# Performance work log

Measured on AMD Instinct MI355X. Metric: run time of the kernel, lower is better.

Reference implementation:

```python
import jax, jax.numpy as jnp
import numpy as np
from jax import lax

V, E, H, K = 50257, 256, 256, 3
T, B, S = 1024, 32, 1024


def setup_inputs() -> dict:
    key = jax.random.key(0)
    ks = jax.random.split(key, 10)
    inp = {
        "source": jax.random.randint(ks[0], (T, B), 0, V),
        "target": jax.random.randint(ks[1], (T, B), 0, V),
        "enc_attn": jax.random.normal(ks[2], (B, S, H), jnp.float32),
        "source_seq_out": jax.random.normal(ks[3], (B, S, 2 * H), jnp.float32),
        "emb": jax.random.normal(ks[4], (V, E), jnp.float32) * 0.02,
        "affine_w": jax.random.normal(ks[5], (2 * H, E), jnp.float32) * 0.02,
        "affine_b": jnp.zeros((2 * H,), jnp.float32),
        "conv_w": jax.random.normal(ks[6], (2 * H, 1, K, 2 * H), jnp.float32) * 0.02,
        "conv_b": jnp.zeros((2 * H,), jnp.float32),
        "map_w": jax.random.normal(ks[7], (2 * H, H), jnp.float32) * 0.02,
        "map_b": jnp.zeros((2 * H,), jnp.float32),
    }
    return inp


def reference(source, target, enc_attn, source_seq_out, emb, affine_w, affine_b,
              conv_w, conv_b, map_w, map_b):
    # source is unused by the original forward (kept for signature fidelity)
    x = emb[target]                                   # [T, B, E]
    x = x @ affine_w.T + affine_b                     # [T, B, 2H]
    x = jnp.transpose(x, (1, 0, 2))                   # [B, T, 2H]  (.t() swaps dims 0,1)
    x = x[:, None, :, :]                              # [B, 1, T, 2H]
    # conv2d: out_ch=2H, kernel=(K, 2H), padding=(K-1, 0) -> [B, 2H, T+K-1, 1]
    y = lax.conv_general_dilated(
        x, conv_w, window_strides=(1, 1),
        padding=((K - 1, K - 1), (0, 0)),
        dimension_numbers=("NCHW", "OIHW", "NCHW"))
    y = y + conv_b[None, :, None, None]
    y = y[:, :, : y.shape[2] - K, :]                  # narrow -> length L = T - 1 (faithful)
    y = jax.nn.relu(y)
    y = jnp.transpose(y[..., 0], (0, 2, 1))           # [B, L, 2H]
    A, Bg = y[..., :H], y[..., H:]                    # GLU split
    dec_attn = A * jax.nn.softmax(Bg, axis=-1)        # [B, L, H]
    dec_attn2 = dec_attn @ map_w.T + map_b            # [B, L, 2H]
    scores = jnp.einsum("blh,bsh->bls", dec_attn, enc_attn)   # [B, L, S]
    attn = jax.nn.softmax(scores, axis=-1)
    attns = jnp.einsum("bls,bsd->bld", attn, source_seq_out)  # [B, L, 2H]
    return dec_attn2 + attns
```

## Files before the change

kernel.cpp:

```cpp
#include <hip/hip_runtime.h>
#include <stdint.h>


typedef __bf16 bf16x8_t __attribute__((ext_vector_type(8)));
typedef float  f32x4_t  __attribute__((ext_vector_type(4)));

#define DEV __device__ __forceinline__

DEV unsigned short f2bf(float f) {
  union { float f; unsigned u; } v; v.f = f;
  unsigned r = v.u + 0x7fffu + ((v.u >> 16) & 1u);
  return (unsigned short)(r >> 16);
}
DEV float bf2f(unsigned short u) {
  union { unsigned u; float f; } v; v.u = ((unsigned)u) << 16;
  return v.f;
}

DEV void gload_lds16(const void* g, void* l) {
  __builtin_amdgcn_global_load_lds((const __attribute__((address_space(1))) void*)g,
                                   (__attribute__((address_space(3))) void*)l, 16, 0, 0);
}

__global__ void zero_k(unsigned short* p) { p[threadIdx.x] = 0; }

__global__ __launch_bounds__(256) void zero_rows_k(float* p) {
  int i = (blockIdx.x * 256 + threadIdx.x) * 4;
  *(float4*)(p + i) = make_float4(0.f, 0.f, 0.f, 0.f);
}

__global__ __launch_bounds__(256) void cvt_bf16_k(const float* __restrict__ src,
                                                  unsigned short* __restrict__ dst,
                                                  int n) {
  int i = (blockIdx.x * 256 + threadIdx.x) * 4;
  if (i >= n) return;
  float4 v = *(const float4*)(src + i);
  ushort4 o;
  o.x = f2bf(v.x); o.y = f2bf(v.y); o.z = f2bf(v.z); o.w = f2bf(v.w);
  *(ushort4*)(dst + i) = o;
}

__global__ __launch_bounds__(256) void cvt_transpose_v_k(const float* __restrict__ src,
                                                         unsigned short* __restrict__ dst) {
  __shared__ float tile[32][33];
  int b = blockIdx.z, s0 = blockIdx.x * 32, d0 = blockIdx.y * 32;
  int tx = threadIdx.x & 31, ty = threadIdx.x >> 5;
  const float* p = src + ((size_t)b * 1024 + s0) * 512 + d0;
  for (int r = ty; r < 32; r += 8) tile[r][tx] = p[(size_t)r * 512 + tx];
  __syncthreads();
  unsigned short* q = dst + ((size_t)b * 512 + d0) * 1024 + s0;
  for (int r = ty; r < 32; r += 8) q[(size_t)r * 1024 + tx] = f2bf(tile[tx][r]);
}

__global__ __launch_bounds__(256) void embed_affine_k(const int* __restrict__ tgt,
                                                      const float* __restrict__ emb,
                                                      const unsigned short* __restrict__ awb,
                                                      const float* __restrict__ ab,
                                                      unsigned short* __restrict__ X) {
  constexpr int AP = 264;
  __shared__ unsigned short xs[32 * AP];
  const int r0 = blockIdx.x * 32;
  const int tid = threadIdx.x;
  for (int idx = tid; idx < 32 * 64; idx += 256) {
    int r = idx >> 6, c4 = (idx & 63) * 4;
    int row = tgt[r0 + r];
    float4 v = *(const float4*)&emb[(size_t)row * 256 + c4];
    ushort4 o;
    o.x = f2bf(v.x); o.y = f2bf(v.y); o.z = f2bf(v.z); o.w = f2bf(v.w);
    *(ushort4*)&xs[r * AP + c4] = o;
  }
  __syncthreads();
  const int lane = tid & 63, w = tid >> 6, q = lane >> 4, ln = lane & 15;
  f32x4_t acc[2][8];
#pragma unroll
  for (int mt = 0; mt < 2; ++mt)
#pragma unroll
    for (int nt = 0; nt < 8; ++nt) acc[mt][nt] = (f32x4_t){0.f, 0.f, 0.f, 0.f};
  for (int kk = 0; kk < 256; kk += 32) {
    bf16x8_t a[2], bb[8];
#pragma unroll
    for (int mt = 0; mt < 2; ++mt)
      a[mt] = *(const bf16x8_t*)(xs + (mt * 16 + ln) * AP + kk + q * 8);
#pragma unroll
    for (int nt = 0; nt < 8; ++nt) {
      int n = ((w * 8 + nt) << 4) + ln;
      bb[nt] = *(const bf16x8_t*)(awb + ((size_t)n << 8) + kk + q * 8);
    }
#pragma unroll
    for (int mt = 0; mt < 2; ++mt)
#pragma unroll
      for (int nt = 0; nt < 8; ++nt)
        acc[mt][nt] = __builtin_amdgcn_mfma_f32_16x16x32_bf16(a[mt], bb[nt], acc[mt][nt], 0, 0, 0);
  }
#pragma unroll
  for (int nt = 0; nt < 8; ++nt) {
    const int o = ((w * 8 + nt) << 4) + ln;
    const float bias = ab[o];
#pragma unroll
    for (int mt = 0; mt < 2; ++mt)
#pragma unroll
      for (int r = 0; r < 4; ++r) {
        int rid = r0 + mt * 16 + q * 4 + r;
        int t = rid >> 5, b = rid & 31;
        X[(((size_t)(b * 1024 + t)) << 9) + o] = f2bf(acc[mt][nt][r] + bias);
      }
  }
}

DEV void cstage(unsigned short* AsB, unsigned short* BsB,
                const unsigned short* __restrict__ X,
                const unsigned short* __restrict__ Wc,
                const unsigned short* __restrict__ zbuf,
                int b, int l0, int n0, int t, int w, int srow, int scolg) {
  const int kk = t << 5;
  const int i  = kk >> 9;
  const int c0 = kk & 511;
  {
    const int lr = l0 + srow + i - 2;
    const unsigned short* sp = (lr < 0)
        ? (zbuf + scolg * 8)
        : (X + (((size_t)(b * 1024 + lr)) << 9) + c0 + scolg * 8);
    gload_lds16(sp, AsB + w * 512);
  }
  {
    const int lr = l0 + 64 + srow + i - 2;
    gload_lds16(X + (((size_t)(b * 1024 + lr)) << 9) + c0 + scolg * 8,
                AsB + 2048 + w * 512);
  }
  gload_lds16(Wc + (size_t)(n0 + srow) * 1536 + kk + scolg * 8, BsB + w * 512);
  gload_lds16(Wc + (size_t)(n0 + 64 + srow) * 1536 + kk + scolg * 8,
              BsB + 2048 + w * 512);
}

__global__ __launch_bounds__(256) void conv_gemm_k(const unsigned short* __restrict__ X,
                                                   const unsigned short* __restrict__ Wc,
                                                   const float* __restrict__ cb,
                                                   const unsigned short* __restrict__ zbuf,
                                                   unsigned short* __restrict__ Y) {
  __shared__ unsigned short As[2][4096];
  __shared__ unsigned short Bs[2][4096];
  const int bid = blockIdx.x;
  const int mtile = bid >> 2;
  const int b  = mtile >> 3;
  const int l0 = (mtile & 7) << 7;
  const int n0 = (bid & 3) << 7;
  const int tid = threadIdx.x;
  const int w = tid >> 6, lane = tid & 63, q = lane >> 4, ln = lane & 15;
  const int wr = w >> 1, wc = w & 1;
  const int srow = tid >> 2, scolg = tid & 3;

  f32x4_t acc[4][4];
#pragma unroll
  for (int mt = 0; mt < 4; ++mt)
#pragma unroll
    for (int nt = 0; nt < 4; ++nt) acc[mt][nt] = (f32x4_t){0.f, 0.f, 0.f, 0.f};

  cstage(As[0], Bs[0], X, Wc, zbuf, b, l0, n0, 0, w, srow, scolg);
  __syncthreads();

  for (int t = 0; t < 48; ++t) {
    const int cur = t & 1;
    if (t < 47)
      cstage(As[cur ^ 1], Bs[cur ^ 1], X, Wc, zbuf, b, l0, n0, t + 1, w, srow, scolg);
    const unsigned short* Ab = As[cur];
    const unsigned short* Bb = Bs[cur];
    bf16x8_t af[4], bf[4];
#pragma unroll
    for (int x = 0; x < 4; ++x) {
      af[x] = *(const bf16x8_t*)(Ab + (wr * 64 + x * 16 + ln) * 32 + q * 8);
      bf[x] = *(const bf16x8_t*)(Bb + (wc * 64 + x * 16 + ln) * 32 + q * 8);
    }
#pragma unroll
    for (int mt = 0; mt < 4; ++mt)
#pragma unroll
      for (int nt = 0; nt < 4; ++nt)
        acc[mt][nt] = __builtin_amdgcn_mfma_f32_16x16x32_bf16(af[mt], bf[nt], acc[mt][nt], 0, 0, 0);
    __syncthreads();
  }

#pragma unroll
  for (int nt = 0; nt < 4; ++nt) {
    const int o = n0 + wc * 64 + nt * 16 + ln;
    const float bias = cb[o];
#pragma unroll
    for (int mt = 0; mt < 4; ++mt)
#pragma unroll
      for (int r = 0; r < 4; ++r) {
        const int l = l0 + wr * 64 + mt * 16 + q * 4 + r;
        float v = acc[mt][nt][r] + bias;
        Y[(((size_t)b * 1024 + l) << 9) + o] = f2bf(v > 0.f ? v : 0.f);
      }
  }
}

__global__ __launch_bounds__(256) void glu_k(const unsigned short* __restrict__ Y,
                                             unsigned short* __restrict__ dec) {
  const int row = blockIdx.x * 4 + (threadIdx.x >> 6);
  const int lane = threadIdx.x & 63;
  const unsigned short* p = Y + ((size_t)row << 9);
  ushort4 av = *(const ushort4*)(p + lane * 4);
  ushort4 gv = *(const ushort4*)(p + 256 + lane * 4);
  float e0 = __expf(bf2f(gv.x)), e1 = __expf(bf2f(gv.y));
  float e2 = __expf(bf2f(gv.z)), e3 = __expf(bf2f(gv.w));
  float s = e0 + e1 + e2 + e3;
#pragma unroll
  for (int off = 32; off > 0; off >>= 1) s += __shfl_xor(s, off);
  float inv = 1.f / s;
  ushort4 o;
  o.x = f2bf(bf2f(av.x) * e0 * inv);
  o.y = f2bf(bf2f(av.y) * e1 * inv);
  o.z = f2bf(bf2f(av.z) * e2 * inv);
  o.w = f2bf(bf2f(av.w) * e3 * inv);
  *(ushort4*)(dec + ((size_t)row << 8) + lane * 4) = o;
}

DEV void gstage(unsigned short* AsB, unsigned short* BsB,
                const unsigned short* __restrict__ Arow,
                const unsigned short* __restrict__ Brow,
                int strideA, int strideB, int kk, int w, int srow, int scolg) {
  gload_lds16(Arow + (size_t)srow * strideA + kk + scolg * 8, AsB + w * 512);
  gload_lds16(Arow + (size_t)(64 + srow) * strideA + kk + scolg * 8,
              AsB + 2048 + w * 512);
  gload_lds16(Brow + (size_t)srow * strideB + kk + scolg * 8, BsB + w * 512);
  gload_lds16(Brow + (size_t)(64 + srow) * strideB + kk + scolg * 8,
              BsB + 2048 + w * 512);
}

__global__ __launch_bounds__(256) void attn_s_k(const unsigned short* __restrict__ dec,
                                                const unsigned short* __restrict__ enc,
                                                unsigned short* __restrict__ P,
                                                float* __restrict__ rows) {
  __shared__ unsigned short As[2][4096];
  __shared__ unsigned short Bs[2][4096];
  const int bid = blockIdx.x;
  const int wg = ((bid & 7) << 8) + (bid >> 3);
  const int ntile = wg & 7, mtile = wg >> 3;
  const int b = mtile >> 3;
  const int row0 = mtile << 7;
  const int s0 = ntile << 7;
  const int tid = threadIdx.x;
  const int w = tid >> 6, lane = tid & 63, q = lane >> 4, ln = lane & 15;
  const int wr = w >> 1, wc = w & 1;
  const int srow = tid >> 2, scolg = tid & 3;

  const unsigned short* Ab = dec + ((size_t)row0 << 8);
  const unsigned short* Bb = enc + ((size_t)b << 18) + ((size_t)s0 << 8);

  f32x4_t acc[4][4];
#pragma unroll
  for (int mt = 0; mt < 4; ++mt)
#pragma unroll
    for (int nt = 0; nt < 4; ++nt) acc[mt][nt] = (f32x4_t){0.f, 0.f, 0.f, 0.f};

  gstage(As[0], Bs[0], Ab, Bb, 256, 256, 0, w, srow, scolg);
  __syncthreads();

  for (int t = 0; t < 8; ++t) {
    const int cur = t & 1;
    if (t < 7)
      gstage(As[cur ^ 1], Bs[cur ^ 1], Ab, Bb, 256, 256, (t + 1) << 5, w, srow, scolg);
    const unsigned short* Ap = As[cur];
    const unsigned short* Bp = Bs[cur];
    bf16x8_t af[4], bf[4];
#pragma unroll
    for (int x = 0; x < 4; ++x) {
      af[x] = *(const bf16x8_t*)(Ap + (wr * 64 + x * 16 + ln) * 32 + q * 8);
      bf[x] = *(const bf16x8_t*)(Bp + (wc * 64 + x * 16 + ln) * 32 + q * 8);
    }
#pragma unroll
    for (int mt = 0; mt < 4; ++mt)
#pragma unroll
      for (int nt = 0; nt < 4; ++nt)
        acc[mt][nt] = __builtin_amdgcn_mfma_f32_16x16x32_bf16(af[mt], bf[nt], acc[mt][nt], 0, 0, 0);
    __syncthreads();
  }

  float rs[4][4];
#pragma unroll
  for (int mt = 0; mt < 4; ++mt)
#pragma unroll
    for (int r = 0; r < 4; ++r) rs[mt][r] = 0.f;
#pragma unroll
  for (int nt = 0; nt < 4; ++nt) {
    const int col = s0 + wc * 64 + nt * 16 + ln;
#pragma unroll
    for (int mt = 0; mt < 4; ++mt)
#pragma unroll
      for (int r = 0; r < 4; ++r) {
        const int row = row0 + wr * 64 + mt * 16 + q * 4 + r;
        float e = __expf(acc[mt][nt][r]);
        rs[mt][r] += e;
        P[((size_t)row << 10) + col] = f2bf(e);
      }
  }
#pragma unroll
  for (int mt = 0; mt < 4; ++mt)
#pragma unroll
    for (int r = 0; r < 4; ++r) {
      float v = rs[mt][r];
      v += __shfl_xor(v, 1); v += __shfl_xor(v, 2);
      v += __shfl_xor(v, 4); v += __shfl_xor(v, 8);
      if (ln == 0)
        atomicAdd(&rows[row0 + wr * 64 + mt * 16 + q * 4 + r], v);
    }
}

__global__ __launch_bounds__(256) void attn_pv_k(const unsigned short* __restrict__ P,
                                                 const unsigned short* __restrict__ vt,
                                                 const unsigned short* __restrict__ dec,
                                                 const unsigned short* __restrict__ mw,
                                                 const float* __restrict__ rows,
                                                 const float* __restrict__ mb,
                                                 float* __restrict__ out) {
  __shared__ unsigned short As[2][4096];
  __shared__ unsigned short Bs[2][4096];
  const int bid = blockIdx.x;
  const int wg = ((bid & 7) << 7) + (bid >> 3);
  const int ntile = wg & 3, mtile = wg >> 2;
  const int b = mtile >> 3;
  const int row0 = mtile << 7;
  const int d0 = ntile << 7;
  const int tid = threadIdx.x;
  const int w = tid >> 6, lane = tid & 63, q = lane >> 4, ln = lane & 15;
  const int wr = w >> 1, wc = w & 1;
  const int srow = tid >> 2, scolg = tid & 3;

  const unsigned short* A1 = P + ((size_t)row0 << 10);
  const unsigned short* B1 = vt + ((size_t)b << 19) + ((size_t)d0 << 10);
  const unsigned short* A2 = dec + ((size_t)row0 << 8);
  const unsigned short* B2 = mw + ((size_t)d0 << 8);

  float rinv[4][4];
#pragma unroll
  for (int mt = 0; mt < 4; ++mt)
#pragma unroll
    for (int r = 0; r < 4; ++r)
      rinv[mt][r] = 1.f / rows[row0 + wr * 64 + mt * 16 + q * 4 + r];

  f32x4_t acc[4][4];
#pragma unroll
  for (int mt = 0; mt < 4; ++mt)
#pragma unroll
    for (int nt = 0; nt < 4; ++nt) acc[mt][nt] = (f32x4_t){0.f, 0.f, 0.f, 0.f};

  gstage(As[0], Bs[0], A1, B1, 1024, 1024, 0, w, srow, scolg);
  __syncthreads();

  for (int t = 0; t < 40; ++t) {
    const int cur = t & 1;
    if (t < 39) {
      const int tn = t + 1;
      if (tn < 32)
        gstage(As[cur ^ 1], Bs[cur ^ 1], A1, B1, 1024, 1024, tn << 5, w, srow, scolg);
      else
        gstage(As[cur ^ 1], Bs[cur ^ 1], A2, B2, 256, 256, (tn - 32) << 5, w, srow, scolg);
    }
    const unsigned short* Ap = As[cur];
    const unsigned short* Bp = Bs[cur];
    bf16x8_t af[4], bf[4];
#pragma unroll
    for (int x = 0; x < 4; ++x) {
      af[x] = *(const bf16x8_t*)(Ap + (wr * 64 + x * 16 + ln) * 32 + q * 8);
      bf[x] = *(const bf16x8_t*)(Bp + (wc * 64 + x * 16 + ln) * 32 + q * 8);
    }
#pragma unroll
    for (int mt = 0; mt < 4; ++mt)
#pragma unroll
      for (int nt = 0; nt < 4; ++nt)
        acc[mt][nt] = __builtin_amdgcn_mfma_f32_16x16x32_bf16(af[mt], bf[nt], acc[mt][nt], 0, 0, 0);
    if (t == 31) {
#pragma unroll
      for (int mt = 0; mt < 4; ++mt)
#pragma unroll
        for (int nt = 0; nt < 4; ++nt)
#pragma unroll
          for (int r = 0; r < 4; ++r) acc[mt][nt][r] *= rinv[mt][r];
    }
    __syncthreads();
  }

#pragma unroll
  for (int nt = 0; nt < 4; ++nt) {
    const int d = d0 + wc * 64 + nt * 16 + ln;
    const float bias = mb[d];
#pragma unroll
    for (int mt = 0; mt < 4; ++mt)
#pragma unroll
      for (int r = 0; r < 4; ++r) {
        const int row = row0 + wr * 64 + mt * 16 + q * 4 + r;
        const int l = row & 1023;
        if (l < 1023)
          out[((size_t)b * 1023 + l) * 512 + d] = acc[mt][nt][r] + bias;
      }
  }
}

extern "C" void kernel_launch(void* const* d_in, const int* in_sizes, int n_in,
                              void* d_out, int out_size, void* d_ws, size_t ws_size,
                              hipStream_t stream) {
  const int*   target = (const int*)d_in[1];
  const float* enc    = (const float*)d_in[2];
  const float* src    = (const float*)d_in[3];
  const float* emb    = (const float*)d_in[4];
  const float* aw     = (const float*)d_in[5];
  const float* ab     = (const float*)d_in[6];
  const float* cw     = (const float*)d_in[7];
  const float* cb     = (const float*)d_in[8];
  const float* mw     = (const float*)d_in[9];
  const float* mb     = (const float*)d_in[10];
  float* out = (float*)d_out;
  char* ws = (char*)d_ws;

  unsigned short* Xbf  = (unsigned short*)(ws);
  unsigned short* Ybf  = (unsigned short*)(ws + 33554432);
  unsigned short* Pb   = (unsigned short*)(ws);
  unsigned short* dec  = (unsigned short*)(ws + 67108864);
  unsigned short* encb = (unsigned short*)(ws + 83886080);
  unsigned short* vtb  = (unsigned short*)(ws + 100663296);
  unsigned short* wcb  = (unsigned short*)(ws + 134217728);
  float*          rows = (float*)(ws + 134217728);
  unsigned short* mwb  = (unsigned short*)(ws + 135790592);
  unsigned short* awb  = (unsigned short*)(ws + 136052736);

  zero_k<<<1, 512, 0, stream>>>(dec);
  cvt_bf16_k<<<8192, 256, 0, stream>>>(enc, encb, 32 * 1024 * 256);
  cvt_bf16_k<<<768, 256, 0, stream>>>(cw, wcb, 512 * 1536);
  cvt_bf16_k<<<128, 256, 0, stream>>>(mw, mwb, 512 * 256);
  cvt_bf16_k<<<128, 256, 0, stream>>>(aw, awb, 512 * 256);
  cvt_transpose_v_k<<<dim3(32, 16, 32), 256, 0, stream>>>(src, vtb);
  embed_affine_k<<<1024, 256, 0, stream>>>(target, emb, awb, ab, Xbf);
  conv_gemm_k<<<1024, 256, 0, stream>>>(Xbf, wcb, cb, dec, Ybf);
  zero_rows_k<<<32, 256, 0, stream>>>(rows);
  glu_k<<<8192, 256, 0, stream>>>(Ybf, dec);
  attn_s_k<<<2048, 256, 0, stream>>>(dec, encb, Pb, rows);
  attn_pv_k<<<1024, 256, 0, stream>>>(Pb, vtb, dec, mwb, rows, mb, out);
}
```

Before: 452.5 us.

## Triple-buffer GEMM kernels with vmcnt barriers, LDS swizzle, and wider transpose

Replaces the double-buffered LDS staging in the conv, attention-score and PV GEMM kernels with a three-stage ring buffer. Each step waits with partial vmcnt counts instead of a full __syncthreads, so two global-to-LDS loads stay in flight. Adds an XOR swizzle on LDS columns to cut bank conflicts, raises MFMA priority with s_setprio, and remaps conv block indices for L2 locality. The V transpose kernel now uses 64x64 tiles with float4 loads and 16-byte bf16 stores. The extra LDS per block (48KB) may limit occupancy, and the hand-written waitcnt counts must match the number of loads issued per stage exactly.

```diff
diff --git a/kernel.cpp b/kernel.cpp
--- a/kernel.cpp
+++ b/kernel.cpp
@@ -4,6 +4,7 @@
 
 typedef __bf16 bf16x8_t __attribute__((ext_vector_type(8)));
 typedef float  f32x4_t  __attribute__((ext_vector_type(4)));
+typedef unsigned short u16x8 __attribute__((ext_vector_type(8)));
 
 #define DEV __device__ __forceinline__
 
@@ -20,6 +21,38 @@
 DEV void gload_lds16(const void* g, void* l) {
   __builtin_amdgcn_global_load_lds((const __attribute__((address_space(1))) void*)g,
                                    (__attribute__((address_space(3))) void*)l, 16, 0, 0);
+}
+
+DEV void vm_bar8() { asm volatile("s_waitcnt vmcnt(8)" ::: "memory"); __builtin_amdgcn_s_barrier(); }
+DEV void vm_bar4() { asm volatile("s_waitcnt vmcnt(4)" ::: "memory"); __builtin_amdgcn_s_barrier(); }
+DEV void vm_bar0() { asm volatile("s_waitcnt vmcnt(0)" ::: "memory"); __builtin_amdgcn_s_barrier(); }
+DEV void lgkm_bar() { asm volatile("s_waitcnt lgkmcnt(0)" ::: "memory"); __builtin_amdgcn_s_barrier(); }
+
+DEV void stage32(unsigned short* Ld, int tid,
+                 const unsigned short* a0, const unsigned short* a1,
+                 const unsigned short* b0, const unsigned short* b1, int tt) {
+  const int o = tt * 32;
+  gload_lds16(a0 + o, Ld + tid * 8);
+  gload_lds16(a1 + o, Ld + (tid + 256) * 8);
+  gload_lds16(b0 + o, Ld + 4096 + tid * 8);
+  gload_lds16(b1 + o, Ld + 4096 + (tid + 256) * 8);
+}
+
+DEV void gemm_step32(const unsigned short* Ld, int wr, int wc, int ln, int qsw,
+                     f32x4_t (&acc)[4][4]) {
+  bf16x8_t af[4], bff[4];
+#pragma unroll
+  for (int x = 0; x < 4; ++x) {
+    af[x]  = *(const bf16x8_t*)(Ld + (wr * 64 + x * 16 + ln) * 32 + qsw);
+    bff[x] = *(const bf16x8_t*)(Ld + 4096 + (wc * 64 + x * 16 + ln) * 32 + qsw);
+  }
+  __builtin_amdgcn_s_setprio(1);
+#pragma unroll
+  for (int mt = 0; mt < 4; ++mt)
+#pragma unroll
+    for (int nt = 0; nt < 4; ++nt)
+      acc[mt][nt] = __builtin_amdgcn_mfma_f32_16x16x32_bf16(af[mt], bff[nt], acc[mt][nt], 0, 0, 0);
+  __builtin_amdgcn_s_setprio(0);
 }
 
 __global__ void zero_k(unsigned short* p) { p[threadIdx.x] = 0; }
@@ -42,14 +75,30 @@
 
 __global__ __launch_bounds__(256) void cvt_transpose_v_k(const float* __restrict__ src,
                                                          unsigned short* __restrict__ dst) {
-  __shared__ float tile[32][33];
-  int b = blockIdx.z, s0 = blockIdx.x * 32, d0 = blockIdx.y * 32;
-  int tx = threadIdx.x & 31, ty = threadIdx.x >> 5;
+  __shared__ float tile[64][65];
+  const int b = blockIdx.z, s0 = blockIdx.x * 64, d0 = blockIdx.y * 64;
+  const int tid = threadIdx.x;
+  const int cs = (tid & 15) * 4;
+  const int rs = tid >> 4;
   const float* p = src + ((size_t)b * 1024 + s0) * 512 + d0;
-  for (int r = ty; r < 32; r += 8) tile[r][tx] = p[(size_t)r * 512 + tx];
+#pragma unroll
+  for (int rr = 0; rr < 4; ++rr) {
+    const int s = rs + rr * 16;
+    float4 v = *(const float4*)(p + (size_t)s * 512 + cs);
+    tile[s][cs] = v.x; tile[s][cs + 1] = v.y;
+    tile[s][cs + 2] = v.z; tile[s][cs + 3] = v.w;
+  }
   __syncthreads();
-  unsigned short* q = dst + ((size_t)b * 512 + d0) * 1024 + s0;
-  for (int r = ty; r < 32; r += 8) q[(size_t)r * 1024 + tx] = f2bf(tile[tx][r]);
+  const int ch = tid & 7;
+  const int dd0 = tid >> 3;
+#pragma unroll
+  for (int it = 0; it < 2; ++it) {
+    const int dd = dd0 + it * 32;
+    u16x8 o;
+#pragma unroll
+    for (int j = 0; j < 8; ++j) o[j] = f2bf(tile[ch * 8 + j][dd]);
+    *(u16x8*)(dst + ((size_t)b * 512 + d0 + dd) * 1024 + s0 + ch * 8) = o;
+  }
 }
 
 __global__ __launch_bounds__(256) void embed_affine_k(const int* __restrict__ tgt,
@@ -107,47 +156,45 @@
   }
 }
 
-DEV void cstage(unsigned short* AsB, unsigned short* BsB,
-                const unsigned short* __restrict__ X,
-                const unsigned short* __restrict__ Wc,
-                const unsigned short* __restrict__ zbuf,
-                int b, int l0, int n0, int t, int w, int srow, int scolg) {
-  const int kk = t << 5;
-  const int i  = kk >> 9;
-  const int c0 = kk & 511;
-  {
-    const int lr = l0 + srow + i - 2;
-    const unsigned short* sp = (lr < 0)
-        ? (zbuf + scolg * 8)
-        : (X + (((size_t)(b * 1024 + lr)) << 9) + c0 + scolg * 8);
-    gload_lds16(sp, AsB + w * 512);
-  }
-  {
-    const int lr = l0 + 64 + srow + i - 2;
-    gload_lds16(X + (((size_t)(b * 1024 + lr)) << 9) + c0 + scolg * 8,
-                AsB + 2048 + w * 512);
-  }
-  gload_lds16(Wc + (size_t)(n0 + srow) * 1536 + kk + scolg * 8, BsB + w * 512);
-  gload_lds16(Wc + (size_t)(n0 + 64 + srow) * 1536 + kk + scolg * 8,
-              BsB + 2048 + w * 512);
-}
-
-__global__ __launch_bounds__(256) void conv_gemm_k(const unsigned short* __restrict__ X,
-                                                   const unsigned short* __restrict__ Wc,
-                                                   const float* __restrict__ cb,
-                                                   const unsigned short* __restrict__ zbuf,
-                                                   unsigned short* __restrict__ Y) {
-  __shared__ unsigned short As[2][4096];
-  __shared__ unsigned short Bs[2][4096];
+__global__ __launch_bounds__(256, 3) void conv_gemm_k(const unsigned short* __restrict__ X,
+                                                      const unsigned short* __restrict__ Wc,
+                                                      const float* __restrict__ cb,
+                                                      const unsigned short* __restrict__ zbuf,
+                                                      unsigned short* __restrict__ Y) {
+  __shared__ unsigned short tb[3][8192];
   const int bid = blockIdx.x;
-  const int mtile = bid >> 2;
+  const int mtile = ((bid >> 5) << 3) | (bid & 7);
+  const int ntile = (bid >> 3) & 3;
   const int b  = mtile >> 3;
   const int l0 = (mtile & 7) << 7;
-  const int n0 = (bid & 3) << 7;
+  const int n0 = ntile << 7;
   const int tid = threadIdx.x;
   const int w = tid >> 6, lane = tid & 63, q = lane >> 4, ln = lane & 15;
   const int wr = w >> 1, wc = w & 1;
-  const int srow = tid >> 2, scolg = tid & 3;
+  const int qsw = (q ^ (ln & 3)) << 3;
+
+  const int r0g = tid >> 2, r1g = (tid + 256) >> 2;
+  const int cg = tid & 3;
+  const int c0g = ((cg ^ (r0g & 3)) << 3);
+  const int c1g = ((cg ^ (r1g & 3)) << 3);
+
+  const unsigned short* Xb = X + ((size_t)b << 19);
+  const int lr0 = l0 + r0g - 2;
+  const int lr1 = l0 + r1g - 2;
+  const int tmin0 = (lr0 >= 0) ? 0 : (lr0 == -1 ? 16 : 32);
+  const unsigned short* a0 = Xb + ((long)lr0 * 512 + c0g);
+  const unsigned short* a1 = Xb + ((long)lr1 * 512 + c1g);
+  const unsigned short* b0 = Wc + (size_t)(n0 + r0g) * 1536 + c0g;
+  const unsigned short* b1 = Wc + (size_t)(n0 + r1g) * 1536 + c1g;
+
+  auto STG = [&](unsigned short* Ld, int tt) {
+    const int o = tt * 32;
+    const unsigned short* sA0 = (tt >= tmin0) ? (a0 + o) : (zbuf + c0g);
+    gload_lds16(sA0, Ld + tid * 8);
+    gload_lds16(a1 + o, Ld + (tid + 256) * 8);
+    gload_lds16(b0 + o, Ld + 4096 + tid * 8);
+    gload_lds16(b1 + o, Ld + 4096 + (tid + 256) * 8);
+  };
 
   f32x4_t acc[4][4];
 #pragma unroll
@@ -155,27 +202,17 @@
 #pragma unroll
     for (int nt = 0; nt < 4; ++nt) acc[mt][nt] = (f32x4_t){0.f, 0.f, 0.f, 0.f};
 
-  cstage(As[0], Bs[0], X, Wc, zbuf, b, l0, n0, 0, w, srow, scolg);
-  __syncthreads();
+  unsigned short *p0 = tb[0], *p1 = tb[1], *p2 = tb[2];
+  STG(p0, 0);
+  STG(p1, 1);
 
   for (int t = 0; t < 48; ++t) {
-    const int cur = t & 1;
-    if (t < 47)
-      cstage(As[cur ^ 1], Bs[cur ^ 1], X, Wc, zbuf, b, l0, n0, t + 1, w, srow, scolg);
-    const unsigned short* Ab = As[cur];
-    const unsigned short* Bb = Bs[cur];
-    bf16x8_t af[4], bf[4];
-#pragma unroll
-    for (int x = 0; x < 4; ++x) {
-      af[x] = *(const bf16x8_t*)(Ab + (wr * 64 + x * 16 + ln) * 32 + q * 8);
-      bf[x] = *(const bf16x8_t*)(Bb + (wc * 64 + x * 16 + ln) * 32 + q * 8);
-    }
-#pragma unroll
-    for (int mt = 0; mt < 4; ++mt)
-#pragma unroll
-      for (int nt = 0; nt < 4; ++nt)
-        acc[mt][nt] = __builtin_amdgcn_mfma_f32_16x16x32_bf16(af[mt], bf[nt], acc[mt][nt], 0, 0, 0);
-    __syncthreads();
+    if (t + 2 < 48) { STG(p2, t + 2); vm_bar8(); }
+    else if (t + 1 < 48) vm_bar4();
+    else vm_bar0();
+    gemm_step32(p0, wr, wc, ln, qsw, acc);
+    lgkm_bar();
+    unsigned short* tmp = p0; p0 = p1; p1 = p2; p2 = tmp;
   }
 
 #pragma unroll
@@ -214,24 +251,11 @@
   *(ushort4*)(dec + ((size_t)row << 8) + lane * 4) = o;
 }
 
-DEV void gstage(unsigned short* AsB, unsigned short* BsB,
-                const unsigned short* __restrict__ Arow,
-                const unsigned short* __restrict__ Brow,
-                int strideA, int strideB, int kk, int w, int srow, int scolg) {
-  gload_lds16(Arow + (size_t)srow * strideA + kk + scolg * 8, AsB + w * 512);
-  gload_lds16(Arow + (size_t)(64 + srow) * strideA + kk + scolg * 8,
-              AsB + 2048 + w * 512);
-  gload_lds16(Brow + (size_t)srow * strideB + kk + scolg * 8, BsB + w * 512);
-  gload_lds16(Brow + (size_t)(64 + srow) * strideB + kk + scolg * 8,
-              BsB + 2048 + w * 512);
-}
-
-__global__ __launch_bounds__(256) void attn_s_k(const unsigned short* __restrict__ dec,
-                                                const unsigned short* __restrict__ enc,
-                                                unsigned short* __restrict__ P,
-                                                float* __restrict__ rows) {
-  __shared__ unsigned short As[2][4096];
-  __shared__ unsigned short Bs[2][4096];
+__global__ __launch_bounds__(256, 3) void attn_s_k(const unsigned short* __restrict__ dec,
+                                                   const unsigned short* __restrict__ enc,
+                                                   unsigned short* __restrict__ P,
+                                                   float* __restrict__ rows) {
+  __shared__ unsigned short tb[3][8192];
   const int bid = blockIdx.x;
   const int wg = ((bid & 7) << 8) + (bid >> 3);
   const int ntile = wg & 7, mtile = wg >> 3;
@@ -241,10 +265,19 @@
   const int tid = threadIdx.x;
   const int w = tid >> 6, lane = tid & 63, q = lane >> 4, ln = lane & 15;
   const int wr = w >> 1, wc = w & 1;
-  const int srow = tid >> 2, scolg = tid & 3;
+  const int qsw = (q ^ (ln & 3)) << 3;
+
+  const int r0g = tid >> 2, r1g = (tid + 256) >> 2;
+  const int cg = tid & 3;
+  const int c0g = ((cg ^ (r0g & 3)) << 3);
+  const int c1g = ((cg ^ (r1g & 3)) << 3);
 
   const unsigned short* Ab = dec + ((size_t)row0 << 8);
   const unsigned short* Bb = enc + ((size_t)b << 18) + ((size_t)s0 << 8);
+  const unsigned short* a0 = Ab + (size_t)r0g * 256 + c0g;
+  const unsigned short* a1 = Ab + (size_t)r1g * 256 + c1g;
+  const unsigned short* b0 = Bb + (size_t)r0g * 256 + c0g;
+  const unsigned short* b1 = Bb + (size_t)r1g * 256 + c1g;
 
   f32x4_t acc[4][4];
 #pragma unroll
@@ -252,27 +285,17 @@
 #pragma unroll
     for (int nt = 0; nt < 4; ++nt) acc[mt][nt] = (f32x4_t){0.f, 0.f, 0.f, 0.f};
 
-  gstage(As[0], Bs[0], Ab, Bb, 256, 256, 0, w, srow, scolg);
-  __syncthreads();
+  unsigned short *p0 = tb[0], *p1 = tb[1], *p2 = tb[2];
+  stage32(p0, tid, a0, a1, b0, b1, 0);
+  stage32(p1, tid, a0, a1, b0, b1, 1);
 
   for (int t = 0; t < 8; ++t) {
-    const int cur = t & 1;
-    if (t < 7)
-      gstage(As[cur ^ 1], Bs[cur ^ 1], Ab, Bb, 256, 256, (t + 1) << 5, w, srow, scolg);
-    const unsigned short* Ap = As[cur];
-    const unsigned short* Bp = Bs[cur];
-    bf16x8_t af[4], bf[4];
-#pragma unroll
-    for (int x = 0; x < 4; ++x) {
-      af[x] = *(const bf16x8_t*)(Ap + (wr * 64 + x * 16 + ln) * 32 + q * 8);
-      bf[x] = *(const bf16x8_t*)(Bp + (wc * 64 + x * 16 + ln) * 32 + q * 8);
-    }
-#pragma unroll
-    for (int mt = 0; mt < 4; ++mt)
-#pragma unroll
-      for (int nt = 0; nt < 4; ++nt)
-        acc[mt][nt] = __builtin_amdgcn_mfma_f32_16x16x32_bf16(af[mt], bf[nt], acc[mt][nt], 0, 0, 0);
-    __syncthreads();
+    if (t + 2 < 8) { stage32(p2, tid, a0, a1, b0, b1, t + 2); vm_bar8(); }
+    else if (t + 1 < 8) vm_bar4();
+    else vm_bar0();
+    gemm_step32(p0, wr, wc, ln, qsw, acc);
+    lgkm_bar();
+    unsigned short* tmp = p0; p0 = p1; p1 = p2; p2 = tmp;
   }
 
   float rs[4][4];
@@ -305,15 +328,14 @@
     }
 }
 
-__global__ __launch_bounds__(256) void attn_pv_k(const unsigned short* __restrict__ P,
-                                                 const unsigned short* __restrict__ vt,
-                                                 const unsigned short* __restrict__ dec,
-                                                 const unsigned short* __restrict__ mw,
-                                                 const float* __restrict__ rows,
-                                                 const float* __restrict__ mb,
-                                                 float* __restrict__ out) {
-  __shared__ unsigned short As[2][4096];
-  __shared__ unsigned short Bs[2][4096];
+__global__ __launch_bounds__(256, 3) void attn_pv_k(const unsigned short* __restrict__ P,
+                                                    const unsigned short* __restrict__ vt,
+                                                    const unsigned short* __restrict__ dec,
+                                                    const unsigned short* __restrict__ mw,
+                                                    const float* __restrict__ rows,
+                                                    const float* __restrict__ mb,
+                                                    float* __restrict__ out) {
+  __shared__ unsigned short tb[3][8192];
   const int bid = blockIdx.x;
   const int wg = ((bid & 7) << 7) + (bid >> 3);
   const int ntile = wg & 3, mtile = wg >> 2;
@@ -323,12 +345,30 @@
   const int tid = threadIdx.x;
   const int w = tid >> 6, lane = tid & 63, q = lane >> 4, ln = lane & 15;
   const int wr = w >> 1, wc = w & 1;
-  const int srow = tid >> 2, scolg = tid & 3;
+  const int qsw = (q ^ (ln & 3)) << 3;
+
+  const int r0g = tid >> 2, r1g = (tid + 256) >> 2;
+  const int cg = tid & 3;
+  const int c0g = ((cg ^ (r0g & 3)) << 3);
+  const int c1g = ((cg ^ (r1g & 3)) << 3);
 
   const unsigned short* A1 = P + ((size_t)row0 << 10);
   const unsigned short* B1 = vt + ((size_t)b << 19) + ((size_t)d0 << 10);
   const unsigned short* A2 = dec + ((size_t)row0 << 8);
   const unsigned short* B2 = mw + ((size_t)d0 << 8);
+  const unsigned short* a10 = A1 + (size_t)r0g * 1024 + c0g;
+  const unsigned short* a11 = A1 + (size_t)r1g * 1024 + c1g;
+  const unsigned short* b10 = B1 + (size_t)r0g * 1024 + c0g;
+  const unsigned short* b11 = B1 + (size_t)r1g * 1024 + c1g;
+  const unsigned short* a20 = A2 + (size_t)r0g * 256 + c0g;
+  const unsigned short* a21 = A2 + (size_t)r1g * 256 + c1g;
+  const unsigned short* b20 = B2 + (size_t)r0g * 256 + c0g;
+  const unsigned short* b21 = B2 + (size_t)r1g * 256 + c1g;
+
+  auto STG = [&](unsigned short* Ld, int tt) {
+    if (tt < 32) stage32(Ld, tid, a10, a11, b10, b11, tt);
+    else         stage32(Ld, tid, a20, a21, b20, b21, tt - 32);
+  };
 
   float rinv[4][4];
 #pragma unroll
@@ -343,40 +383,30 @@
 #pragma unroll
     for (int nt = 0; nt < 4; ++nt) acc[mt][nt] = (f32x4_t){0.f, 0.f, 0.f, 0.f};
 
-  gstage(As[0], Bs[0], A1, B1, 1024, 1024, 0, w, srow, scolg);
-  __syncthreads();
-
-  for (int t = 0; t < 40; ++t) {
-    const int cur = t & 1;
-    if (t < 39) {
-      const int tn = t + 1;
-      if (tn < 32)
-        gstage(As[cur ^ 1], Bs[cur ^ 1], A1, B1, 1024, 1024, tn << 5, w, srow, scolg);
-      else
-        gstage(As[cur ^ 1], Bs[cur ^ 1], A2, B2, 256, 256, (tn - 32) << 5, w, srow, scolg);
-    }
-    const unsigned short* Ap = As[cur];
-    const unsigned short* Bp = Bs[cur];
-    bf16x8_t af[4], bf[4];
-#pragma unroll
-    for (int x = 0; x < 4; ++x) {
-      af[x] = *(const bf16x8_t*)(Ap + (wr * 64 + x * 16 + ln) * 32 + q * 8);
-      bf[x] = *(const bf16x8_t*)(Bp + (wc * 64 + x * 16 + ln) * 32 + q * 8);
-    }
-#pragma unroll
-    for (int mt = 0; mt < 4; ++mt)
-#pragma unroll
-      for (int nt = 0; nt < 4; ++nt)
-        acc[mt][nt] = __builtin_amdgcn_mfma_f32_16x16x32_bf16(af[mt], bf[nt], acc[mt][nt], 0, 0, 0);
-    if (t == 31) {
-#pragma unroll
-      for (int mt = 0; mt < 4; ++mt)
-#pragma unroll
-        for (int nt = 0; nt < 4; ++nt)
-#pragma unroll
-          for (int r = 0; r < 4; ++r) acc[mt][nt][r] *= rinv[mt][r];
-    }
-    __syncthreads();
+  unsigned short *p0 = tb[0], *p1 = tb[1], *p2 = tb[2];
+  STG(p0, 0);
+  STG(p1, 1);
+
+  for (int t = 0; t < 32; ++t) {
+    STG(p2, t + 2); vm_bar8();
+    gemm_step32(p0, wr, wc, ln, qsw, acc);
+    lgkm_bar();
+    unsigned short* tmp = p0; p0 = p1; p1 = p2; p2 = tmp;
+  }
+#pragma unroll
+  for (int mt = 0; mt < 4; ++mt)
+#pragma unroll
+    for (int nt = 0; nt < 4; ++nt)
+#pragma unroll
+      for (int r = 0; r < 4; ++r) acc[mt][nt][r] *= rinv[mt][r];
+
+  for (int t = 32; t < 40; ++t) {
+    if (t + 2 < 40) { STG(p2, t + 2); vm_bar8(); }
+    else if (t + 1 < 40) vm_bar4();
+    else vm_bar0();
+    gemm_step32(p0, wr, wc, ln, qsw, acc);
+    lgkm_bar();
+    unsigned short* tmp = p0; p0 = p1; p1 = p2; p2 = tmp;
   }
 
 #pragma unroll
@@ -427,7 +457,7 @@
   cvt_bf16_k<<<768, 256, 0, stream>>>(cw, wcb, 512 * 1536);
   cvt_bf16_k<<<128, 256, 0, stream>>>(mw, mwb, 512 * 256);
   cvt_bf16_k<<<128, 256, 0, stream>>>(aw, awb, 512 * 256);
-  cvt_transpose_v_k<<<dim3(32, 16, 32), 256, 0, stream>>>(src, vtb);
+  cvt_transpose_v_k<<<dim3(16, 8, 32), 256, 0, stream>>>(src, vtb);
   embed_affine_k<<<1024, 256, 0, stream>>>(target, emb, awb, ab, Xbf);
   conv_gemm_k<<<1024, 256, 0, stream>>>(Xbf, wcb, cb, dec, Ybf);
   zero_rows_k<<<32, 256, 0, stream>>>(rows);
```

New measurement: 415.6 us. 1.09x faster.
